# Kernel tuning notes

Hardware: AMD Instinct MI355X
Metric: run time of the kernel (lower is better)

Reference implementation:

```python
import jax, jax.numpy as jnp
import numpy as np

VOCAB, T, IN, H, L = 32000, 4096, 512, 256, 2


def setup_inputs() -> dict:
    key = jax.random.key(0)
    ks = jax.random.split(key, 32)
    inp = {}
    inp["tokens"] = jax.random.randint(ks[0], (T,), 0, VOCAB)
    inp["emb"] = jax.random.normal(ks[1], (VOCAB, IN), dtype=jnp.float32) * 0.02
    i = 2
    for d in ("f", "b"):
        for l in range(L):
            in_l = IN if l == 0 else H
            inp[f"{d}_Wih{l}"] = jax.random.normal(ks[i], (4 * H, in_l), dtype=jnp.float32) * 0.05; i += 1
            inp[f"{d}_Whh{l}"] = jax.random.normal(ks[i], (4 * H, H), dtype=jnp.float32) * 0.05; i += 1
            inp[f"{d}_bih{l}"] = jnp.zeros((4 * H,), dtype=jnp.float32)
            inp[f"{d}_bhh{l}"] = jnp.zeros((4 * H,), dtype=jnp.float32)
    return inp


def _lstm_layer(x_seq, Wih, Whh, bih, bhh):
    # x_seq: [T, in]; torch.nn.LSTMCell gate order: i, f, g, o
    Hh = Whh.shape[1]
    b = bih + bhh
    def step(carry, x):
        h, c = carry
        g = x @ Wih.T + h @ Whh.T + b           # [4H]
        i_, f_, g_, o_ = jnp.split(g, 4)
        c = jax.nn.sigmoid(f_) * c + jax.nn.sigmoid(i_) * jnp.tanh(g_)
        h = jax.nn.sigmoid(o_) * jnp.tanh(c)
        return (h, c), h
    z = jnp.zeros((Hh,), x_seq.dtype)
    (h, c), hs = jax.lax.scan(step, (z, z), x_seq)
    return hs, h, c                              # [T,H], [H], [H]


def _run_dir(x_seq, params):
    finals = []
    h_seq = x_seq
    for (Wih, Whh, bih, bhh) in params:
        h_seq, h, c = _lstm_layer(h_seq, Wih, Whh, bih, bhh)
        finals.append((c, h))
    return h_seq, finals


def reference(tokens, emb,
              f_Wih0, f_Whh0, f_bih0, f_bhh0, f_Wih1, f_Whh1, f_bih1, f_bhh1,
              b_Wih0, b_Whh0, b_bih0, b_bhh0, b_Wih1, b_Whh1, b_bih1, b_bhh1):
    x = emb[tokens]                              # [T, IN] embedding lookup
    fparams = [(f_Wih0, f_Whh0, f_bih0, f_bhh0), (f_Wih1, f_Whh1, f_bih1, f_bhh1)]
    bparams = [(b_Wih0, b_Whh0, b_bih0, b_bhh0), (b_Wih1, b_Whh1, b_bih1, b_bhh1)]
    f_out, f_fin = _run_dir(x, fparams)          # forward over sequence
    b_out_rev, b_fin = _run_dir(x[::-1], bparams)  # backward over reversed sequence
    b_out = b_out_rev[::-1]
    outputs = jnp.concatenate([f_out, b_out], axis=-1)  # [T, 2H]
    cell_memories = jnp.stack([jnp.stack([f_fin[l][0], b_fin[l][0]]) for l in range(L)])  # [L,2,H]
    hidden_states = jnp.stack([jnp.stack([f_fin[l][1], b_fin[l][1]]) for l in range(L)])  # [L,2,H]
    return cell_memories, hidden_states, outputs
```

## Files before the change

### kernel.cpp

```cpp
#include <hip/hip_runtime.h>
#include <math.h>

#define T_SEQ 4096

__device__ __forceinline__ float sigmoidf_(float x) {
  return 1.0f / (1.0f + expf(-x));
}

__device__ __forceinline__ unsigned long long pack_h(int tag, float h) {
  return ((unsigned long long)(unsigned)tag << 32) |
         (unsigned long long)__float_as_uint(h);
}

__device__ __forceinline__ unsigned long long ld_fast(const unsigned long long* p) {
  unsigned long long v;
  asm volatile("global_load_dwordx2 %0, %1, off sc1\n\ts_waitcnt vmcnt(0)"
               : "=v"(v) : "v"(p) : "memory");
  return v;
}
__device__ __forceinline__ unsigned long long ld_mall(const unsigned long long* p) {
  unsigned long long v;
  asm volatile("global_load_dwordx2 %0, %1, off sc0 sc1\n\ts_waitcnt vmcnt(0)"
               : "=v"(v) : "v"(p) : "memory");
  return v;
}
__device__ __forceinline__ void st_pub(unsigned long long* p, unsigned long long v) {
  asm volatile("global_store_dwordx2 %0, %1, off\n\t"
               "global_store_dwordx2 %0, %1, off sc0 sc1"
               :: "v"(p), "v"(v) : "memory");
}
__device__ __forceinline__ float poll_h(const unsigned long long* p, unsigned want) {
  int it = 0;
  for (;;) {
    unsigned long long v = ((it & 3) == 3) ? ld_mall(p) : ld_fast(p);
    if ((unsigned)(v >> 32) == want) return __uint_as_float((unsigned)v);
    ++it;
  }
}

__device__ __forceinline__ void bar() {
  asm volatile("s_waitcnt lgkmcnt(0)" ::: "memory");
  __builtin_amdgcn_s_barrier();
  asm volatile("" ::: "memory");
}

#define DECL_W8(p) float4 p##0, p##1, p##2, p##3, p##4, p##5, p##6, p##7
#define LOAD_W8(p, src) do { const float4* _s = (const float4*)(src); \
  p##0=_s[0]; p##1=_s[1]; p##2=_s[2]; p##3=_s[3]; \
  p##4=_s[4]; p##5=_s[5]; p##6=_s[6]; p##7=_s[7]; } while (0)
#define PIN4(v4) asm volatile("" : "+v"((v4).x), "+v"((v4).y), \
                                   "+v"((v4).z), "+v"((v4).w))
#define PIN_W8(p) do { PIN4(p##0); PIN4(p##1); PIN4(p##2); PIN4(p##3); \
  PIN4(p##4); PIN4(p##5); PIN4(p##6); PIN4(p##7); } while (0)
#define FMA4(acc, W_, H_) do { acc = fmaf((W_).x, (H_).x, acc); \
  acc = fmaf((W_).y, (H_).y, acc); acc = fmaf((W_).z, (H_).z, acc); \
  acc = fmaf((W_).w, (H_).w, acc); } while (0)

__global__ void gather_emb(const int* __restrict__ tokens,
                           const float4* __restrict__ emb4,
                           float4* __restrict__ X4) {
  int i = blockIdx.x * 256 + threadIdx.x;
  int t = i >> 7;
  int q = i & 127;
  X4[i] = emb4[(long)tokens[t] * 128 + q];
}

__global__ __launch_bounds__(256) void gemm_proj(
    const float* __restrict__ Xf, const float* __restrict__ Xb, int revb,
    const float* __restrict__ Wf, const float* __restrict__ Wb,
    const float* __restrict__ bihf, const float* __restrict__ bhhf,
    const float* __restrict__ bihb, const float* __restrict__ bhhb,
    float* __restrict__ Pf, float* __restrict__ Pb, int K)
{
  const int dirb = blockIdx.z;
  const float* X  = dirb ? Xb : Xf;
  const float* W  = dirb ? Wb : Wf;
  const float* bih = dirb ? bihb : bihf;
  const float* bhh = dirb ? bhhb : bhhf;
  float* Pp = dirb ? Pb : Pf;
  const int rev = dirb ? revb : 0;

  const int bn = blockIdx.x;
  const int bm = blockIdx.y;
  const int tid = threadIdx.x;
  const int tx = tid & 15, ty = tid >> 4;

  __shared__ float Xs[16][68];
  __shared__ float Ws[16][68];

  float acc[4][4] = {{0.f}};

  const int lrow = tid >> 2;
  const int lk4  = (tid & 3) * 4;
  const int xrow = bm * 64 + lrow;
  const int xsrc = rev ? (4095 - xrow) : xrow;
  const float* xptr = X + (long)xsrc * K + lk4;
  const float* wptr = W + (long)(bn * 64 + lrow) * K + lk4;

  for (int k0 = 0; k0 < K; k0 += 16) {
    float4 xv = *(const float4*)(xptr + k0);
    float4 wv = *(const float4*)(wptr + k0);
    __syncthreads();
    Xs[lk4 + 0][lrow] = xv.x; Xs[lk4 + 1][lrow] = xv.y;
    Xs[lk4 + 2][lrow] = xv.z; Xs[lk4 + 3][lrow] = xv.w;
    Ws[lk4 + 0][lrow] = wv.x; Ws[lk4 + 1][lrow] = wv.y;
    Ws[lk4 + 2][lrow] = wv.z; Ws[lk4 + 3][lrow] = wv.w;
    __syncthreads();
    #pragma unroll
    for (int kk = 0; kk < 16; ++kk) {
      float4 a = *(const float4*)(&Xs[kk][ty * 4]);
      float4 b = *(const float4*)(&Ws[kk][tx * 4]);
      acc[0][0] = fmaf(a.x, b.x, acc[0][0]); acc[0][1] = fmaf(a.x, b.y, acc[0][1]);
      acc[0][2] = fmaf(a.x, b.z, acc[0][2]); acc[0][3] = fmaf(a.x, b.w, acc[0][3]);
      acc[1][0] = fmaf(a.y, b.x, acc[1][0]); acc[1][1] = fmaf(a.y, b.y, acc[1][1]);
      acc[1][2] = fmaf(a.y, b.z, acc[1][2]); acc[1][3] = fmaf(a.y, b.w, acc[1][3]);
      acc[2][0] = fmaf(a.z, b.x, acc[2][0]); acc[2][1] = fmaf(a.z, b.y, acc[2][1]);
      acc[2][2] = fmaf(a.z, b.z, acc[2][2]); acc[2][3] = fmaf(a.z, b.w, acc[2][3]);
      acc[3][0] = fmaf(a.w, b.x, acc[3][0]); acc[3][1] = fmaf(a.w, b.y, acc[3][1]);
      acc[3][2] = fmaf(a.w, b.z, acc[3][2]); acc[3][3] = fmaf(a.w, b.w, acc[3][3]);
    }
  }

  const int c0 = bn * 64 + tx * 4;
  #pragma unroll
  for (int i = 0; i < 4; ++i) {
    const int r = bm * 64 + ty * 4 + i;
    float4 o4;
    o4.x = acc[i][0] + bih[c0 + 0] + bhh[c0 + 0];
    o4.y = acc[i][1] + bih[c0 + 1] + bhh[c0 + 1];
    o4.z = acc[i][2] + bih[c0 + 2] + bhh[c0 + 2];
    o4.w = acc[i][3] + bih[c0 + 3] + bhh[c0 + 3];
    *(float4*)(&Pp[(long)r * 1024 + c0]) = o4;
  }
}

__global__ __launch_bounds__(512, 1) void lstm_fused(
    const float* __restrict__ P0f, const float* __restrict__ P0b,
    const float* __restrict__ Whh0f, const float* __restrict__ Whh0b,
    const float* __restrict__ Wih1f, const float* __restrict__ Whh1f,
    const float* __restrict__ bih1f, const float* __restrict__ bhh1f,
    const float* __restrict__ Wih1b, const float* __restrict__ Whh1b,
    const float* __restrict__ bih1b, const float* __restrict__ bhh1b,
    float* __restrict__ out,
    unsigned long long* __restrict__ ring0,
    unsigned long long* __restrict__ h1x,
    int* __restrict__ claim)
{
  const int t = threadIdx.x;

  __shared__ int s_dir, s_sub;
  __shared__ float hx[512];
  __shared__ float part[8 * 264];

  int hwv;
  asm volatile("s_getreg_b32 %0, hwreg(HW_REG_XCC_ID)" : "=s"(hwv));
  const int myxcd = hwv & 7;
  if (t == 0) {
    int* cnt  = claim;
    int* xdir = claim + 16;
    int r = atomicAdd(&cnt[myxcd], 1);
    if (r == 0) {
      int dslot = atomicAdd(&cnt[8], 1);
      atomicExch(&xdir[myxcd], (dslot < 2) ? (dslot + 1) : 3);
    }
    int dv;
    do { dv = atomicAdd(&xdir[myxcd], 0); } while (dv == 0);
    s_dir = (dv <= 2 && r < 12) ? (dv - 1) : -1;
    s_sub = r;
  }
  __syncthreads();
  if (s_dir < 0) return;
  const int d   = s_dir;
  const int sub = s_sub;

  unsigned long long* ring = ring0 + (long)d * T_SEQ * 256;

  if (sub < 4) {
    const int w = sub;
    const int wbase = w * 64;
    const float* __restrict__ P = d ? P0b : P0f;
    const float* __restrict__ W = d ? Whh0b : Whh0f;

    const int kb = t >> 6;
    const int jg = t & 63;

    DECL_W8(wa); DECL_W8(wb); DECL_W8(wc); DECL_W8(wd);
    LOAD_W8(wa, W + (long)(0 * 256 + wbase + jg) * 256 + kb * 32);
    LOAD_W8(wb, W + (long)(1 * 256 + wbase + jg) * 256 + kb * 32);
    LOAD_W8(wc, W + (long)(2 * 256 + wbase + jg) * 256 + kb * 32);
    LOAD_W8(wd, W + (long)(3 * 256 + wbase + jg) * 256 + kb * 32);
    PIN_W8(wa); PIN_W8(wb); PIN_W8(wc); PIN_W8(wd);

    const long pj = (long)((t & 3) * 256 + wbase + (t >> 2));

    float pv_cur = 0.0f, c_prev = 0.0f;
    if (t < 256) { pv_cur = P[pj]; hx[t] = 0.0f; }

    for (int s = 0; s < T_SEQ; ++s) {
      if (s > 0 && t >= 256 && t < 448) {
        const int q = t - 256;
        const int pcell = (q < wbase) ? q : q + 64;
        hx[pcell] = poll_h(ring + (long)(s - 1) * 256 + pcell, (unsigned)s);
      }
      float pv_next = 0.0f;
      if (t < 256 && s + 1 < T_SEQ) pv_next = P[(long)(s + 1) * 1024 + pj];
      bar();

      float a0 = 0.f, a1 = 0.f, a2 = 0.f, a3 = 0.f;
      const float4* h4 = (const float4*)&hx[kb * 32];
      #define L0STEP(q) do { float4 hv = h4[q]; FMA4(a0, wa##q, hv); \
        FMA4(a1, wb##q, hv); FMA4(a2, wc##q, hv); FMA4(a3, wd##q, hv); } while (0)
      L0STEP(0); L0STEP(1); L0STEP(2); L0STEP(3);
      L0STEP(4); L0STEP(5); L0STEP(6); L0STEP(7);
      #undef L0STEP
      float4 av; av.x = a0; av.y = a1; av.z = a2; av.w = a3;
      *(float4*)(&part[kb * 264 + jg * 4]) = av;
      bar();

      if (t < 256) {
        float g = pv_cur;
        #pragma unroll
        for (int q = 0; q < 8; ++q) g += part[q * 264 + t];
        float act = ((t & 3) == 2) ? tanhf(g) : sigmoidf_(g);
        float y  = __shfl_xor(act, 1);
        float zx = __shfl_xor(act, 2);
        float zy = __shfl_xor(y, 2);
        const bool l1b = (t & 1), h1b = (t & 2);
        float i_ = h1b ? (l1b ? zy : zx) : (l1b ? y : act);
        float f_ = h1b ? (l1b ? zx : zy) : (l1b ? act : y);
        float g_ = h1b ? (l1b ? y : act) : (l1b ? zy : zx);
        float o_ = h1b ? (l1b ? act : y) : (l1b ? zx : zy);
        float c = f_ * c_prev + i_ * g_;
        c_prev = c;
        float h = o_ * tanhf(c);
        if ((t & 3) == 0) {
          const int gc = wbase + (t >> 2);
          hx[gc] = h;
          st_pub(ring + (long)s * 256 + gc, pack_h(s + 1, h));
          if (s == T_SEQ - 1) {
            out[d * 256 + gc] = c;
            out[1024 + d * 256 + gc] = h;
          }
        }
        pv_cur = pv_next;
      }
    }
  } else {
    const int w1 = sub - 4;
    const int wbase1 = w1 * 32;
    const float* __restrict__ Wih = d ? Wih1b : Wih1f;
    const float* __restrict__ Whh = d ? Whh1b : Whh1f;
    const float* __restrict__ bih = d ? bih1b : bih1f;
    const float* __restrict__ bhh = d ? bhh1b : bhh1f;
    unsigned long long* slot = h1x + d * 512;
    float* hout = d ? (out + 2048 + (long)4095 * 512 + 256) : (out + 2048);
    const long hstr = d ? -512 : 512;

    const int kb = t >> 6;
    const int jg = t & 63;

    const int m0 = jg * 2, m1 = m0 + 1;
    const int j0 = (m0 & 3) * 256 + wbase1 + (m0 >> 2);
    const int j1 = (m1 & 3) * 256 + wbase1 + (m1 >> 2);
    const float* s0 = (kb < 4) ? (Wih + (long)j0 * 256 + kb * 64)
                               : (Whh + (long)j0 * 256 + (kb - 4) * 64);
    const float* s1 = (kb < 4) ? (Wih + (long)j1 * 256 + kb * 64)
                               : (Whh + (long)j1 * 256 + (kb - 4) * 64);
    DECL_W8(ua); DECL_W8(ub); DECL_W8(uc); DECL_W8(ud);
    LOAD_W8(ua, s0); LOAD_W8(ub, s0 + 32);
    LOAD_W8(uc, s1); LOAD_W8(ud, s1 + 32);
    PIN_W8(ua); PIN_W8(ub); PIN_W8(uc); PIN_W8(ud);

    float bsum = 0.0f, c_prev = 0.0f;
    if (t < 128) {
      const int j = (t & 3) * 256 + wbase1 + (t >> 2);
      bsum = bih[j] + bhh[j];
      if ((t & 3) == 0) hx[256 + wbase1 + (t >> 2)] = 0.0f;
    }

    for (int s = 0; s < T_SEQ; ++s) {
      if (t >= 128 && t < 384) {
        const int c0_ = t - 128;
        hx[c0_] = poll_h(ring + (long)s * 256 + c0_, (unsigned)(s + 1));
      } else {
        int q1 = -1;
        if (t < 128) { if ((t & 3) != 0) q1 = (t >> 2) * 3 + (t & 3) - 1; }
        else q1 = 96 + (t - 384);
        if (q1 >= 0) {
          const int pc1 = (q1 < wbase1) ? q1 : q1 + 32;
          hx[256 + pc1] = poll_h(slot + ((s + 1) & 1) * 256 + pc1, (unsigned)s);
        }
      }
      bar();

      float a0 = 0.f, a1 = 0.f;
      const float4* h4 = (const float4*)&hx[kb * 64];
      #define L1STEPA(q) do { float4 hv = h4[q];     FMA4(a0, ua##q, hv); \
        FMA4(a1, uc##q, hv); } while (0)
      #define L1STEPB(q) do { float4 hv = h4[8 + q]; FMA4(a0, ub##q, hv); \
        FMA4(a1, ud##q, hv); } while (0)
      L1STEPA(0); L1STEPA(1); L1STEPA(2); L1STEPA(3);
      L1STEPA(4); L1STEPA(5); L1STEPA(6); L1STEPA(7);
      L1STEPB(0); L1STEPB(1); L1STEPB(2); L1STEPB(3);
      L1STEPB(4); L1STEPB(5); L1STEPB(6); L1STEPB(7);
      #undef L1STEPA
      #undef L1STEPB
      float2 av2; av2.x = a0; av2.y = a1;
      *(float2*)(&part[kb * 264 + jg * 2]) = av2;
      bar();

      if (t < 128) {
        float g = bsum;
        #pragma unroll
        for (int q = 0; q < 8; ++q) g += part[q * 264 + t];
        float act = ((t & 3) == 2) ? tanhf(g) : sigmoidf_(g);
        float y  = __shfl_xor(act, 1);
        float zx = __shfl_xor(act, 2);
        float zy = __shfl_xor(y, 2);
        const bool l1b = (t & 1), h1b = (t & 2);
        float i_ = h1b ? (l1b ? zy : zx) : (l1b ? y : act);
        float f_ = h1b ? (l1b ? zx : zy) : (l1b ? act : y);
        float g_ = h1b ? (l1b ? y : act) : (l1b ? zy : zx);
        float o_ = h1b ? (l1b ? act : y) : (l1b ? zx : zy);
        float c = f_ * c_prev + i_ * g_;
        c_prev = c;
        float h = o_ * tanhf(c);
        if ((t & 3) == 0) {
          const int gc = wbase1 + (t >> 2);
          hx[256 + gc] = h;
          st_pub(&slot[(s & 1) * 256 + gc], pack_h(s + 1, h));
          hout[(long)s * hstr + gc] = h;
          if (s == T_SEQ - 1) {
            out[512 + d * 256 + gc] = c;
            out[1024 + 512 + d * 256 + gc] = h;
          }
        }
      }
    }
  }
}

extern "C" void kernel_launch(void* const* d_in, const int* in_sizes, int n_in,
                              void* d_out, int out_size, void* d_ws, size_t ws_size,
                              hipStream_t stream) {
  const int*   tokens = (const int*)d_in[0];
  const float* emb    = (const float*)d_in[1];
  const float* fWih0 = (const float*)d_in[2];
  const float* fWhh0 = (const float*)d_in[3];
  const float* fbih0 = (const float*)d_in[4];
  const float* fbhh0 = (const float*)d_in[5];
  const float* fWih1 = (const float*)d_in[6];
  const float* fWhh1 = (const float*)d_in[7];
  const float* fbih1 = (const float*)d_in[8];
  const float* fbhh1 = (const float*)d_in[9];
  const float* bWih0 = (const float*)d_in[10];
  const float* bWhh0 = (const float*)d_in[11];
  const float* bbih0 = (const float*)d_in[12];
  const float* bbhh0 = (const float*)d_in[13];
  const float* bWih1 = (const float*)d_in[14];
  const float* bWhh1 = (const float*)d_in[15];
  const float* bbih1 = (const float*)d_in[16];
  const float* bbhh1 = (const float*)d_in[17];

  float* out = (float*)d_out;
  float* ws  = (float*)d_ws;

  float* X   = ws;
  float* P0f = ws + 4194304;
  float* P0b = ws + 8388608;
  unsigned long long* ring0 = (unsigned long long*)ws;
  unsigned long long* h1x   = (unsigned long long*)(ws + 12582912);
  int* claim = (int*)(ws + 12584960);

  gather_emb<<<2048, 256, 0, stream>>>(tokens, (const float4*)emb, (float4*)X);

  gemm_proj<<<dim3(16, 64, 2), 256, 0, stream>>>(
      X, X, 1, fWih0, bWih0, fbih0, fbhh0, bbih0, bbhh0, P0f, P0b, 512);

  hipMemsetAsync(ring0, 0, (size_t)2 * T_SEQ * 256 * sizeof(unsigned long long), stream);
  hipMemsetAsync(h1x, 0, 1024 * sizeof(unsigned long long), stream);
  hipMemsetAsync(claim, 0, 32 * sizeof(int), stream);

  lstm_fused<<<dim3(768), 512, 0, stream>>>(
      P0f, P0b, fWhh0, bWhh0,
      fWih1, fWhh1, fbih1, fbhh1,
      bWih1, bWhh1, bbih1, bbhh1,
      out, ring0, h1x, claim);
}
```

Measured before the change: 7.227 ms.

## Split h publication into fast double-buffered L2 slots plus a MALL truth copy

Each published hidden value is now written to a small double-buffered fast array with a plain store and separately to the ring or slot with a system-coherent store. Consumers poll the fast copy with an sc0 load and fall back to the coherent copy every fourth iteration. The layer-1 poller of layer-0 values also detects a stale overwrite in the fast buffer and switches to the truth copy. The aim is to cut cross-workgroup handoff latency on the serial recurrence, at the cost of an extra store per value and cache-coherence assumptions within one XCD. The new h1fast buffer is never zeroed.

Result: slower. 8.078 ms (+11.8%).

```diff
diff --git a/kernel.cpp b/kernel.cpp
--- a/kernel.cpp
+++ b/kernel.cpp
@@ -12,9 +12,9 @@
          (unsigned long long)__float_as_uint(h);
 }
 
-__device__ __forceinline__ unsigned long long ld_fast(const unsigned long long* p) {
+__device__ __forceinline__ unsigned long long ld_l2(const unsigned long long* p) {
   unsigned long long v;
-  asm volatile("global_load_dwordx2 %0, %1, off sc1\n\ts_waitcnt vmcnt(0)"
+  asm volatile("global_load_dwordx2 %0, %1, off sc0\n\ts_waitcnt vmcnt(0)"
                : "=v"(v) : "v"(p) : "memory");
   return v;
 }
@@ -24,17 +24,44 @@
                : "=v"(v) : "v"(p) : "memory");
   return v;
 }
-__device__ __forceinline__ void st_pub(unsigned long long* p, unsigned long long v) {
-  asm volatile("global_store_dwordx2 %0, %1, off\n\t"
-               "global_store_dwordx2 %0, %1, off sc0 sc1"
+__device__ __forceinline__ void st_fast(unsigned long long* p, unsigned long long v) {
+  asm volatile("global_store_dwordx2 %0, %1, off"
                :: "v"(p), "v"(v) : "memory");
 }
-__device__ __forceinline__ float poll_h(const unsigned long long* p, unsigned want) {
+__device__ __forceinline__ void st_mall(unsigned long long* p, unsigned long long v) {
+  asm volatile("global_store_dwordx2 %0, %1, off sc0 sc1"
+               :: "v"(p), "v"(v) : "memory");
+}
+
+__device__ __forceinline__ float poll_dual(const unsigned long long* fast_p,
+                                           const unsigned long long* truth_p,
+                                           unsigned want) {
   int it = 0;
   for (;;) {
-    unsigned long long v = ((it & 3) == 3) ? ld_mall(p) : ld_fast(p);
+    unsigned long long v = ((it & 3) == 3) ? ld_mall(truth_p) : ld_l2(fast_p);
     if ((unsigned)(v >> 32) == want) return __uint_as_float((unsigned)v);
     ++it;
+  }
+}
+__device__ __forceinline__ float poll_h0(const unsigned long long* fast_p,
+                                         const unsigned long long* truth_p,
+                                         unsigned want) {
+  int it = 0;
+  for (;;) {
+    if ((it & 3) == 3) {
+      unsigned long long v = ld_mall(truth_p);
+      if ((unsigned)(v >> 32) == want) return __uint_as_float((unsigned)v);
+    } else {
+      unsigned long long v = ld_l2(fast_p);
+      unsigned tag = (unsigned)(v >> 32);
+      if (tag == want) return __uint_as_float((unsigned)v);
+      if (tag > want) break;
+    }
+    ++it;
+  }
+  for (;;) {
+    unsigned long long v = ld_mall(truth_p);
+    if ((unsigned)(v >> 32) == want) return __uint_as_float((unsigned)v);
   }
 }
 
@@ -144,6 +171,8 @@
     float* __restrict__ out,
     unsigned long long* __restrict__ ring0,
     unsigned long long* __restrict__ h1x,
+    unsigned long long* __restrict__ l0fast,
+    unsigned long long* __restrict__ h1fast,
     int* __restrict__ claim)
 {
   const int t = threadIdx.x;
@@ -174,6 +203,8 @@
   const int sub = s_sub;
 
   unsigned long long* ring = ring0 + (long)d * T_SEQ * 256;
+  unsigned long long* l0f  = l0fast + (long)d * 512;
+  unsigned long long* h1f  = h1fast + (long)d * 512;
 
   if (sub < 4) {
     const int w = sub;
@@ -200,7 +231,8 @@
       if (s > 0 && t >= 256 && t < 448) {
         const int q = t - 256;
         const int pcell = (q < wbase) ? q : q + 64;
-        hx[pcell] = poll_h(ring + (long)(s - 1) * 256 + pcell, (unsigned)s);
+        hx[pcell] = poll_dual(l0f + ((s - 1) & 1) * 256 + pcell,
+                              ring + (long)(s - 1) * 256 + pcell, (unsigned)s);
       }
       float pv_next = 0.0f;
       if (t < 256 && s + 1 < T_SEQ) pv_next = P[(long)(s + 1) * 1024 + pj];
@@ -233,16 +265,18 @@
         float c = f_ * c_prev + i_ * g_;
         c_prev = c;
         float h = o_ * tanhf(c);
+        pv_cur = pv_next;
         if ((t & 3) == 0) {
           const int gc = wbase + (t >> 2);
           hx[gc] = h;
-          st_pub(ring + (long)s * 256 + gc, pack_h(s + 1, h));
+          unsigned long long pk = pack_h(s + 1, h);
+          st_fast(l0f + (s & 1) * 256 + gc, pk);
+          st_mall(ring + (long)s * 256 + gc, pk);
           if (s == T_SEQ - 1) {
             out[d * 256 + gc] = c;
             out[1024 + d * 256 + gc] = h;
           }
         }
-        pv_cur = pv_next;
       }
     }
   } else {
@@ -281,14 +315,17 @@
     for (int s = 0; s < T_SEQ; ++s) {
       if (t >= 128 && t < 384) {
         const int c0_ = t - 128;
-        hx[c0_] = poll_h(ring + (long)s * 256 + c0_, (unsigned)(s + 1));
+        hx[c0_] = poll_h0(l0f + (s & 1) * 256 + c0_,
+                          ring + (long)s * 256 + c0_, (unsigned)(s + 1));
       } else {
         int q1 = -1;
         if (t < 128) { if ((t & 3) != 0) q1 = (t >> 2) * 3 + (t & 3) - 1; }
         else q1 = 96 + (t - 384);
         if (q1 >= 0) {
           const int pc1 = (q1 < wbase1) ? q1 : q1 + 32;
-          hx[256 + pc1] = poll_h(slot + ((s + 1) & 1) * 256 + pc1, (unsigned)s);
+          hx[256 + pc1] = poll_dual(h1f + ((s + 1) & 1) * 256 + pc1,
+                                    slot + ((s + 1) & 1) * 256 + pc1,
+                                    (unsigned)s);
         }
       }
       bar();
@@ -328,7 +365,9 @@
         if ((t & 3) == 0) {
           const int gc = wbase1 + (t >> 2);
           hx[256 + gc] = h;
-          st_pub(&slot[(s & 1) * 256 + gc], pack_h(s + 1, h));
+          unsigned long long pk = pack_h(s + 1, h);
+          st_fast(h1f + (s & 1) * 256 + gc, pk);
+          st_mall(&slot[(s & 1) * 256 + gc], pk);
           hout[(long)s * hstr + gc] = h;
           if (s == T_SEQ - 1) {
             out[512 + d * 256 + gc] = c;
@@ -368,9 +407,11 @@
   float* X   = ws;
   float* P0f = ws + 4194304;
   float* P0b = ws + 8388608;
-  unsigned long long* ring0 = (unsigned long long*)ws;
-  unsigned long long* h1x   = (unsigned long long*)(ws + 12582912);
+  unsigned long long* ring0  = (unsigned long long*)ws;
+  unsigned long long* h1x    = (unsigned long long*)(ws + 12582912);
   int* claim = (int*)(ws + 12584960);
+  unsigned long long* l0fast = (unsigned long long*)(ws + 12584992);
+  unsigned long long* h1fast = (unsigned long long*)(ws + 12587040);
 
   gather_emb<<<2048, 256, 0, stream>>>(tokens, (const float4*)emb, (float4*)X);
 
@@ -380,10 +421,11 @@
   hipMemsetAsync(ring0, 0, (size_t)2 * T_SEQ * 256 * sizeof(unsigned long long), stream);
   hipMemsetAsync(h1x, 0, 1024 * sizeof(unsigned long long), stream);
   hipMemsetAsync(claim, 0, 32 * sizeof(int), stream);
+  hipMemsetAsync(l0fast, 0, 2048 * sizeof(unsigned long long), stream);
 
   lstm_fused<<<dim3(768), 512, 0, stream>>>(
       P0f, P0b, fWhh0, bWhh0,
       fWih1, fWhh1, fbih1, fbhh1,
       bWih1, bWhh1, bbih1, bbhh1,
-      out, ring0, h1x, claim);
-}
+      out, ring0, h1x, l0fast, h1fast, claim);
+}
```

## Drop XCD-aware block claiming and poll/publish via MALL-scope only

Applied to the files above, without the earlier changes.

Removes the per-XCD atomic claiming scheme that co-located each direction's 12 blocks on one XCD. The kernel now launches exactly 24 blocks with direction and sub-index taken from blockIdx. Polling and publishing of hidden states now go only through device-coherent (sc0 sc1) loads and stores, with no L2-local fast path. This cuts startup atomics and the 744 idle blocks, but cross-block handoffs may now cross XCDs and pay higher latency on each of the 4096 serial steps.

Measured after the change: 7.064 ms. 2.2% less time.

```diff
diff --git a/kernel.cpp b/kernel.cpp
--- a/kernel.cpp
+++ b/kernel.cpp
@@ -12,29 +12,20 @@
          (unsigned long long)__float_as_uint(h);
 }
 
-__device__ __forceinline__ unsigned long long ld_fast(const unsigned long long* p) {
-  unsigned long long v;
-  asm volatile("global_load_dwordx2 %0, %1, off sc1\n\ts_waitcnt vmcnt(0)"
-               : "=v"(v) : "v"(p) : "memory");
-  return v;
-}
 __device__ __forceinline__ unsigned long long ld_mall(const unsigned long long* p) {
   unsigned long long v;
   asm volatile("global_load_dwordx2 %0, %1, off sc0 sc1\n\ts_waitcnt vmcnt(0)"
                : "=v"(v) : "v"(p) : "memory");
   return v;
 }
-__device__ __forceinline__ void st_pub(unsigned long long* p, unsigned long long v) {
-  asm volatile("global_store_dwordx2 %0, %1, off\n\t"
-               "global_store_dwordx2 %0, %1, off sc0 sc1"
+__device__ __forceinline__ void st_mall(unsigned long long* p, unsigned long long v) {
+  asm volatile("global_store_dwordx2 %0, %1, off sc0 sc1"
                :: "v"(p), "v"(v) : "memory");
 }
-__device__ __forceinline__ float poll_h(const unsigned long long* p, unsigned want) {
-  int it = 0;
+__device__ __forceinline__ float poll_mall(const unsigned long long* p, unsigned want) {
   for (;;) {
-    unsigned long long v = ((it & 3) == 3) ? ld_mall(p) : ld_fast(p);
+    unsigned long long v = ld_mall(p);
     if ((unsigned)(v >> 32) == want) return __uint_as_float((unsigned)v);
-    ++it;
   }
 }
 
@@ -143,35 +134,15 @@
     const float* __restrict__ bih1b, const float* __restrict__ bhh1b,
     float* __restrict__ out,
     unsigned long long* __restrict__ ring0,
-    unsigned long long* __restrict__ h1x,
-    int* __restrict__ claim)
+    unsigned long long* __restrict__ h1x)
 {
-  const int t = threadIdx.x;
-
-  __shared__ int s_dir, s_sub;
+  const int bx = blockIdx.x;
+  const int t  = threadIdx.x;
+  const int d   = bx & 1;
+  const int sub = bx >> 1;
+
   __shared__ float hx[512];
   __shared__ float part[8 * 264];
-
-  int hwv;
-  asm volatile("s_getreg_b32 %0, hwreg(HW_REG_XCC_ID)" : "=s"(hwv));
-  const int myxcd = hwv & 7;
-  if (t == 0) {
-    int* cnt  = claim;
-    int* xdir = claim + 16;
-    int r = atomicAdd(&cnt[myxcd], 1);
-    if (r == 0) {
-      int dslot = atomicAdd(&cnt[8], 1);
-      atomicExch(&xdir[myxcd], (dslot < 2) ? (dslot + 1) : 3);
-    }
-    int dv;
-    do { dv = atomicAdd(&xdir[myxcd], 0); } while (dv == 0);
-    s_dir = (dv <= 2 && r < 12) ? (dv - 1) : -1;
-    s_sub = r;
-  }
-  __syncthreads();
-  if (s_dir < 0) return;
-  const int d   = s_dir;
-  const int sub = s_sub;
 
   unsigned long long* ring = ring0 + (long)d * T_SEQ * 256;
 
@@ -200,7 +171,7 @@
       if (s > 0 && t >= 256 && t < 448) {
         const int q = t - 256;
         const int pcell = (q < wbase) ? q : q + 64;
-        hx[pcell] = poll_h(ring + (long)(s - 1) * 256 + pcell, (unsigned)s);
+        hx[pcell] = poll_mall(ring + (long)(s - 1) * 256 + pcell, (unsigned)s);
       }
       float pv_next = 0.0f;
       if (t < 256 && s + 1 < T_SEQ) pv_next = P[(long)(s + 1) * 1024 + pj];
@@ -233,16 +204,16 @@
         float c = f_ * c_prev + i_ * g_;
         c_prev = c;
         float h = o_ * tanhf(c);
+        pv_cur = pv_next;
         if ((t & 3) == 0) {
           const int gc = wbase + (t >> 2);
           hx[gc] = h;
-          st_pub(ring + (long)s * 256 + gc, pack_h(s + 1, h));
+          st_mall(ring + (long)s * 256 + gc, pack_h(s + 1, h));
           if (s == T_SEQ - 1) {
             out[d * 256 + gc] = c;
             out[1024 + d * 256 + gc] = h;
           }
         }
-        pv_cur = pv_next;
       }
     }
   } else {
@@ -281,14 +252,15 @@
     for (int s = 0; s < T_SEQ; ++s) {
       if (t >= 128 && t < 384) {
         const int c0_ = t - 128;
-        hx[c0_] = poll_h(ring + (long)s * 256 + c0_, (unsigned)(s + 1));
+        hx[c0_] = poll_mall(ring + (long)s * 256 + c0_, (unsigned)(s + 1));
       } else {
         int q1 = -1;
         if (t < 128) { if ((t & 3) != 0) q1 = (t >> 2) * 3 + (t & 3) - 1; }
         else q1 = 96 + (t - 384);
         if (q1 >= 0) {
           const int pc1 = (q1 < wbase1) ? q1 : q1 + 32;
-          hx[256 + pc1] = poll_h(slot + ((s + 1) & 1) * 256 + pc1, (unsigned)s);
+          hx[256 + pc1] = poll_mall(slot + ((s + 1) & 1) * 256 + pc1,
+                                    (unsigned)s);
         }
       }
       bar();
@@ -328,7 +300,7 @@
         if ((t & 3) == 0) {
           const int gc = wbase1 + (t >> 2);
           hx[256 + gc] = h;
-          st_pub(&slot[(s & 1) * 256 + gc], pack_h(s + 1, h));
+          st_mall(&slot[(s & 1) * 256 + gc], pack_h(s + 1, h));
           hout[(long)s * hstr + gc] = h;
           if (s == T_SEQ - 1) {
             out[512 + d * 256 + gc] = c;
@@ -370,7 +342,6 @@
   float* P0b = ws + 8388608;
   unsigned long long* ring0 = (unsigned long long*)ws;
   unsigned long long* h1x   = (unsigned long long*)(ws + 12582912);
-  int* claim = (int*)(ws + 12584960);
 
   gather_emb<<<2048, 256, 0, stream>>>(tokens, (const float4*)emb, (float4*)X);
 
@@ -379,11 +350,10 @@
 
   hipMemsetAsync(ring0, 0, (size_t)2 * T_SEQ * 256 * sizeof(unsigned long long), stream);
   hipMemsetAsync(h1x, 0, 1024 * sizeof(unsigned long long), stream);
-  hipMemsetAsync(claim, 0, 32 * sizeof(int), stream);
-
-  lstm_fused<<<dim3(768), 512, 0, stream>>>(
+
+  lstm_fused<<<dim3(24), 512, 0, stream>>>(
       P0f, P0b, fWhh0, bWhh0,
       fWih1, fWhh1, fbih1, fbhh1,
       bWih1, bWhh1, bbih1, bbhh1,
-      out, ring0, h1x, claim);
-}
+      out, ring0, h1x);
+}
```
